# Performance work log

Hardware: AMD Instinct MI355X
Metric: run time of the kernel (lower is better)

The kernel has to match this reference:

```python
import jax, jax.numpy as jnp
import numpy as np

B, S, D = 4, 2048, 1024   # batch, seq_len, size
K = 4                     # max_choice
A = 2                     # activate_choice (== default forward choices)


def setup_inputs() -> dict:
    key = jax.random.key(0)
    ks = jax.random.split(key, 8)
    sc = 0.02  # weight init scale
    return {
        "x": jax.random.normal(ks[0], (B, S, D), jnp.float32),
        "Wm": jax.random.normal(ks[1], (A, D, D), jnp.float32) * sc,   # Memory expert weights
        "bm": jnp.zeros((A, D), jnp.float32),
        "ln_g": jnp.ones((D,), jnp.float32),                            # shared LayerNorm (self.lim)
        "ln_b": jnp.zeros((D,), jnp.float32),
        "Wg": jax.random.normal(ks[2], (D, K), jnp.float32) * sc,       # Linker gate
        "bg": jnp.zeros((K,), jnp.float32),
        "We": jax.random.normal(ks[3], (K, D, D), jnp.float32) * sc,    # Linker experts
        "be": jnp.zeros((K, D), jnp.float32),
        "Wfit": jax.random.normal(ks[4], ((A + 1) * D, D), jnp.float32) * sc,
        "bfit": jnp.zeros((D,), jnp.float32),
        "choices": A,
    }


def _layer_norm(x, g, b, eps=1e-5):
    m = jnp.mean(x, axis=-1, keepdims=True)
    v = jnp.mean((x - m) ** 2, axis=-1, keepdims=True)
    return (x - m) * jax.lax.rsqrt(v + eps) * g + b


def reference(x, Wm, bm, ln_g, ln_b, Wg, bg, We, be, Wfit, bfit, choices):
    # Triple-nested per-token loop vectorized: the in-place += means each
    # choice's Memory expert sees the x already updated by previous choices,
    # i.e. sequentially over `choices`: x <- x + LN(Memory_c(x)).
    for c in range(choices):
        mem = jnp.einsum('bsd,de->bse', x, Wm[c]) + bm[c]
        x = x + _layer_norm(mem, ln_g, ln_b)

    # Linker: gate over max_choice experts, pick top-`choices`, concat outputs.
    logits = jnp.einsum('bsd,dk->bsk', x, Wg) + bg          # [B,S,K]
    _, idx = jax.lax.top_k(logits, choices)                  # [B,S,A]
    eo = jnp.einsum('bsd,kde->bske', x, We) + be             # [B,S,K,D]
    sel = jnp.take_along_axis(eo, idx[..., None], axis=2)    # [B,S,A,D]
    link = sel.reshape(sel.shape[0], sel.shape[1], -1)       # [B,S,A*D]

    h = jnp.concatenate([link, x], axis=-1)                  # [B,S,(A+1)*D]
    h = jnp.einsum('bsf,fd->bsd', h, Wfit) + bfit
    h = _layer_norm(h, ln_g, ln_b)
    return jax.nn.gelu(h, approximate=False)
```

## Files before the change

### kernel.cpp

```cpp
#include <hip/hip_runtime.h>
#include <hip/hip_bf16.h>
#include <math.h>

typedef __bf16 bf16x8 __attribute__((ext_vector_type(8)));
typedef float  f32x4  __attribute__((ext_vector_type(4)));
typedef unsigned int   u32;
typedef unsigned short u16;
typedef u16 u16x8 __attribute__((ext_vector_type(8)));

#define D_ 1024
#define M_ 8192

static __device__ __forceinline__ u16 f2bf(float f) {
  u32 x = __float_as_uint(f);
  return (u16)((x + 0x7fffu + ((x >> 16) & 1u)) >> 16);
}
static __device__ __forceinline__ float bf2f(u16 s) {
  union { u32 b; float f; } u; u.b = ((u32)s) << 16; return u.f;
}
static __device__ __forceinline__ void gload16(const u16* g, u16* l) {
  __builtin_amdgcn_global_load_lds((const __attribute__((address_space(1))) u32*)g,
                                   (__attribute__((address_space(3))) u32*)l, 16, 0, 0);
}


__global__ __launch_bounds__(256) void pack_A_mem(const float* __restrict__ x, u16* __restrict__ dst) {
  int gid = blockIdx.x * 256 + threadIdx.x;
  int G = gid & 2047;
  int kblk = (gid >> 11) & 31;
  int mblk = gid >> 16;
  int rrow = G >> 3, gp = G & 7;
  int kg = gp ^ (rrow & 7);
  int region = kblk >> 4;
  int k = ((kblk & 15) * 8 + kg) * 8;
  const float* src = x + ((size_t)mblk * 256 + rrow) * D_ + k;
  f32x4 v0 = *reinterpret_cast<const f32x4*>(src);
  f32x4 v1 = *reinterpret_cast<const f32x4*>(src + 4);
  u16x8 o8;
#pragma unroll
  for (int j = 0; j < 4; ++j) {
    u16 h0 = f2bf(v0[j]); o8[j]     = region ? f2bf(v0[j] - bf2f(h0)) : h0;
    u16 h1 = f2bf(v1[j]); o8[4 + j] = region ? f2bf(v1[j] - bf2f(h1)) : h1;
  }
  *reinterpret_cast<u16x8*>(dst + (size_t)gid * 8) = o8;
}

__global__ __launch_bounds__(256) void pack_W_mem(const float* __restrict__ W, u16* __restrict__ dst) {
  __shared__ float tile[64][129];
  int bidx = blockIdx.x;
  int nt = bidx & 7, kt = (bidx >> 3) & 15, c = bidx >> 7;
  const float* Ws = W + ((size_t)c * D_ + kt * 64) * D_ + nt * 128;
#pragma unroll
  for (int rep = 0; rep < 32; ++rep) {
    int idx = rep * 256 + threadIdx.x;
    tile[idx >> 7][idx & 127] = Ws[(size_t)(idx >> 7) * D_ + (idx & 127)];
  }
  __syncthreads();
#pragma unroll
  for (int rep = 0; rep < 8; ++rep) {
    int gi = rep * 256 + threadIdx.x;
    int region = gi >> 10;
    int G = gi & 1023;
    int col = G >> 3, gp = G & 7;
    int kg = gp ^ (col & 7);
    u16x8 o8;
#pragma unroll
    for (int j = 0; j < 8; ++j) {
      float v = tile[kg * 8 + j][col];
      u16 h = f2bf(v);
      o8[j] = region ? f2bf(v - bf2f(h)) : h;
    }
    int kblk = region * 16 + kt;
    size_t off = ((((size_t)c * 8 + nt) * 32 + kblk) * 1024 + col * 8 + gp) * 8;
    *reinterpret_cast<u16x8*>(dst + off) = o8;
  }
}

__global__ __launch_bounds__(256) void pack_W_plain(const float* __restrict__ W, u16* __restrict__ dst, int KBLK) {
  __shared__ float tile[64][129];
  int bidx = blockIdx.x;
  int nt = bidx & 7;
  int t2 = bidx >> 3;
  int kt = t2 % KBLK;
  int e  = t2 / KBLK;
  const float* Ws = W + ((size_t)e * KBLK * 64 + kt * 64) * D_ + nt * 128;
#pragma unroll
  for (int rep = 0; rep < 32; ++rep) {
    int idx = rep * 256 + threadIdx.x;
    tile[idx >> 7][idx & 127] = Ws[(size_t)(idx >> 7) * D_ + (idx & 127)];
  }
  __syncthreads();
#pragma unroll
  for (int rep = 0; rep < 4; ++rep) {
    int gi = rep * 256 + threadIdx.x;
    int col = gi >> 3, gp = gi & 7;
    int kg = gp ^ (col & 7);
    u16x8 o8;
#pragma unroll
    for (int j = 0; j < 8; ++j) o8[j] = f2bf(tile[kg * 8 + j][col]);
    size_t off = ((((size_t)e * 8 + nt) * KBLK + kt) * 1024 + col * 8 + gp) * 8;
    *reinterpret_cast<u16x8*>(dst + off) = o8;
  }
}


__global__ __launch_bounds__(256) void ln1_pack(const float* __restrict__ xin, const float* __restrict__ mem,
                                                const float* __restrict__ bm, const float* __restrict__ g,
                                                const float* __restrict__ b, float* __restrict__ xout,
                                                u16* __restrict__ apack) {
  int row = blockIdx.x, tid = threadIdx.x;
  __shared__ float yrow[1024];
  __shared__ float red[8];
  f32x4 mv = *reinterpret_cast<const f32x4*>(mem + (size_t)row * D_ + tid * 4);
  f32x4 bi = *reinterpret_cast<const f32x4*>(bm + tid * 4);
  float a[4]; float s = 0.f, ss = 0.f;
#pragma unroll
  for (int i = 0; i < 4; ++i) { a[i] = mv[i] + bi[i]; s += a[i]; ss += a[i] * a[i]; }
#pragma unroll
  for (int o = 1; o < 64; o <<= 1) { s += __shfl_xor(s, o); ss += __shfl_xor(ss, o); }
  int wv = tid >> 6, ln = tid & 63;
  if (ln == 0) { red[wv] = s; red[4 + wv] = ss; }
  __syncthreads();
  float S = red[0] + red[1] + red[2] + red[3];
  float SS = red[4] + red[5] + red[6] + red[7];
  float mean = S * (1.f / 1024.f);
  float var = SS * (1.f / 1024.f) - mean * mean;
  float rs = rsqrtf(var + 1e-5f);
  f32x4 g4 = *reinterpret_cast<const f32x4*>(g + tid * 4);
  f32x4 b4 = *reinterpret_cast<const f32x4*>(b + tid * 4);
  f32x4 xv = *reinterpret_cast<const f32x4*>(xin + (size_t)row * D_ + tid * 4);
  f32x4 o4;
#pragma unroll
  for (int i = 0; i < 4; ++i) o4[i] = xv[i] + (a[i] - mean) * rs * g4[i] + b4[i];
  *reinterpret_cast<f32x4*>(xout + (size_t)row * D_ + tid * 4) = o4;
  *reinterpret_cast<f32x4*>(yrow + tid * 4) = o4;
  __syncthreads();
  int region = tid >> 7;
  int q = tid & 127;
  int kblk = region * 16 + (q >> 3);
  int kg = q & 7;
  int rrow = row & 255, mblk = row >> 8;
  const float* ys = yrow + q * 8;
  u16x8 o8;
#pragma unroll
  for (int j = 0; j < 8; ++j) {
    float v = ys[j]; u16 h = f2bf(v);
    o8[j] = region ? f2bf(v - bf2f(h)) : h;
  }
  size_t off = (((size_t)mblk * 32 + kblk) * 2048 + rrow * 8 + (kg ^ (rrow & 7))) * 8;
  *reinterpret_cast<u16x8*>(apack + off) = o8;
}

__global__ __launch_bounds__(256) void ln2_gate_pack(const float* __restrict__ xin, const float* __restrict__ mem,
                                                     const float* __restrict__ bm1, const float* __restrict__ g,
                                                     const float* __restrict__ b, const float* __restrict__ Wg,
                                                     const float* __restrict__ bg, u16* __restrict__ apack,
                                                     u16* __restrict__ hpack, int2* __restrict__ idx) {
  int row = blockIdx.x, tid = threadIdx.x;
  __shared__ float yrow[1024];
  __shared__ float red[8];
  __shared__ float gred[16];
  f32x4 mv = *reinterpret_cast<const f32x4*>(mem + (size_t)row * D_ + tid * 4);
  f32x4 bi = *reinterpret_cast<const f32x4*>(bm1 + tid * 4);
  float a[4]; float s = 0.f, ss = 0.f;
#pragma unroll
  for (int i = 0; i < 4; ++i) { a[i] = mv[i] + bi[i]; s += a[i]; ss += a[i] * a[i]; }
#pragma unroll
  for (int o = 1; o < 64; o <<= 1) { s += __shfl_xor(s, o); ss += __shfl_xor(ss, o); }
  int wv = tid >> 6, ln = tid & 63;
  if (ln == 0) { red[wv] = s; red[4 + wv] = ss; }
  __syncthreads();
  float S = red[0] + red[1] + red[2] + red[3];
  float SS = red[4] + red[5] + red[6] + red[7];
  float mean = S * (1.f / 1024.f);
  float var = SS * (1.f / 1024.f) - mean * mean;
  float rs = rsqrtf(var + 1e-5f);
  f32x4 g4 = *reinterpret_cast<const f32x4*>(g + tid * 4);
  f32x4 b4 = *reinterpret_cast<const f32x4*>(b + tid * 4);
  f32x4 xv = *reinterpret_cast<const f32x4*>(xin + (size_t)row * D_ + tid * 4);
  f32x4 o4;
#pragma unroll
  for (int i = 0; i < 4; ++i) o4[i] = xv[i] + (a[i] - mean) * rs * g4[i] + b4[i];
  *reinterpret_cast<f32x4*>(yrow + tid * 4) = o4;
  float p0 = 0.f, p1 = 0.f, p2 = 0.f, p3 = 0.f;
#pragma unroll
  for (int i = 0; i < 4; ++i) {
    f32x4 w = *reinterpret_cast<const f32x4*>(Wg + (size_t)(tid * 4 + i) * 4);
    p0 += o4[i] * w[0]; p1 += o4[i] * w[1]; p2 += o4[i] * w[2]; p3 += o4[i] * w[3];
  }
#pragma unroll
  for (int o = 1; o < 64; o <<= 1) {
    p0 += __shfl_xor(p0, o); p1 += __shfl_xor(p1, o);
    p2 += __shfl_xor(p2, o); p3 += __shfl_xor(p3, o);
  }
  if (ln == 0) { gred[wv * 4] = p0; gred[wv * 4 + 1] = p1; gred[wv * 4 + 2] = p2; gred[wv * 4 + 3] = p3; }
  __syncthreads();
  if (tid == 0) {
    float lg[4];
#pragma unroll
    for (int c = 0; c < 4; ++c) lg[c] = gred[c] + gred[4 + c] + gred[8 + c] + gred[12 + c] + bg[c];
    int i0 = 0; float v0 = lg[0];
#pragma unroll
    for (int k = 1; k < 4; ++k) if (lg[k] > v0) { v0 = lg[k]; i0 = k; }
    int i1 = -1; float v1 = -3.4e38f;
#pragma unroll
    for (int k = 0; k < 4; ++k) if (k != i0 && lg[k] > v1) { v1 = lg[k]; i1 = k; }
    idx[row] = make_int2(i0, i1);
  }
  int q = tid & 127;
  int kblk = q >> 3, kg = q & 7;
  int rrow = row & 255, mblk = row >> 8;
  const float* ys = yrow + q * 8;
  u16x8 o8;
#pragma unroll
  for (int j = 0; j < 8; ++j) o8[j] = f2bf(ys[j]);
  int pos = rrow * 8 + (kg ^ (rrow & 7));
  if (tid < 128) {
    *reinterpret_cast<u16x8*>(apack + (((size_t)mblk * 16 + kblk) * 2048 + pos) * 8) = o8;
  } else {
    *reinterpret_cast<u16x8*>(hpack + (((size_t)mblk * 48 + 32 + kblk) * 2048 + pos) * 8) = o8;
  }
}

__global__ __launch_bounds__(256) void final_ln_gelu(const float* __restrict__ fit, const float* __restrict__ bfit,
                                                     const float* __restrict__ g, const float* __restrict__ b,
                                                     float* __restrict__ out) {
  int row = blockIdx.x, tid = threadIdx.x;
  f32x4 hv = *reinterpret_cast<const f32x4*>(fit + (size_t)row * D_ + tid * 4);
  f32x4 bi = *reinterpret_cast<const f32x4*>(bfit + tid * 4);
  float a[4]; float s = 0.f, ss = 0.f;
#pragma unroll
  for (int i = 0; i < 4; ++i) { a[i] = hv[i] + bi[i]; s += a[i]; ss += a[i] * a[i]; }
#pragma unroll
  for (int o = 1; o < 64; o <<= 1) { s += __shfl_xor(s, o); ss += __shfl_xor(ss, o); }
  __shared__ float red[8];
  int wv = tid >> 6, ln = tid & 63;
  if (ln == 0) { red[wv] = s; red[4 + wv] = ss; }
  __syncthreads();
  float S = red[0] + red[1] + red[2] + red[3];
  float SS = red[4] + red[5] + red[6] + red[7];
  float mean = S * (1.f / 1024.f);
  float var = SS * (1.f / 1024.f) - mean * mean;
  float rs = rsqrtf(var + 1e-5f);
  f32x4 g4 = *reinterpret_cast<const f32x4*>(g + tid * 4);
  f32x4 b4 = *reinterpret_cast<const f32x4*>(b + tid * 4);
  f32x4 o4;
#pragma unroll
  for (int i = 0; i < 4; ++i) {
    float y = (a[i] - mean) * rs * g4[i] + b4[i];
    o4[i] = 0.5f * y * (1.f + erff(y * 0.70710678118654752f));
  }
  *reinterpret_cast<f32x4*>(out + (size_t)row * D_ + tid * 4) = o4;
}

#define MFMA(a, b, c) __builtin_amdgcn_mfma_f32_16x16x32_bf16(a, b, c, 0, 0, 0)

template<int MEMFOLD, int EPI>
__global__ __launch_bounds__(256, 2) void gemm4(const u16* __restrict__ A, const u16* __restrict__ B,
                                                float* __restrict__ C, u16* __restrict__ hp,
                                                const int2* __restrict__ idx, const float* __restrict__ be,
                                                int KIT, int AKB, int BKB) {
  __shared__ __align__(16) u16 lds[16384];
  const int tid = threadIdx.x;
  const int wid = tid >> 6, l = tid & 63;
  const int wm = wid >> 1, wn = wid & 1;
  const int lk = l >> 4, l15 = l & 15;
  const int bid = blockIdx.x;
  const int mblk = bid & 63;
  const int nblk = (bid >> 6) & 7;
  const int e    = bid >> 9;
  const int half = mblk & 1;

  const u16* Ablob = A + (size_t)(mblk >> 1) * AKB * 16384 + (size_t)half * 8192;
  const u16* Bblob = B + ((size_t)e * 8 + nblk) * BKB * 8192;

  f32x4 acc[4][4];
#pragma unroll
  for (int i = 0; i < 4; ++i)
#pragma unroll
    for (int j = 0; j < 4; ++j) acc[i][j] = (f32x4){0.f, 0.f, 0.f, 0.f};

  auto amap = [&](int it) -> int {
    if (!MEMFOLD) return it;
    int kb = (int)((unsigned)it / 3u), sub = it - kb * 3;
    return kb + (sub == 2 ? 16 : 0);
  };
  auto bmap = [&](int it) -> int {
    if (!MEMFOLD) return it;
    int kb = (int)((unsigned)it / 3u), sub = it - kb * 3;
    return kb + (sub == 1 ? 16 : 0);
  };

  auto ldA = [&](int mi, int ks) -> bf16x8 {
    int r = wm * 64 + mi * 16 + l15;
    int gp = (ks * 4 + lk) ^ (r & 7);
    return *reinterpret_cast<const bf16x8*>(&lds[(r * 8 + gp) * 8]);
  };
  auto ldB = [&](int ni, int ks) -> bf16x8 {
    int c = wn * 64 + ni * 16 + l15;
    int gp = (ks * 4 + lk) ^ (c & 7);
    return *reinterpret_cast<const bf16x8*>(&lds[8192 + (c * 8 + gp) * 8]);
  };

  for (int t = 0; t < KIT; ++t) {
    const u16* As = Ablob + (size_t)amap(t) * 16384;
    const u16* Bs = Bblob + (size_t)bmap(t) * 8192;
#pragma unroll
    for (int i = 0; i < 4; ++i) {
      int u = i * 256 + tid;
      gload16(As + (size_t)u * 8, &lds[u * 8]);
      gload16(Bs + (size_t)u * 8, &lds[8192 + u * 8]);
    }
    __syncthreads();
#pragma unroll
    for (int ks = 0; ks < 2; ++ks) {
      bf16x8 A0 = ldA(0, ks), A1 = ldA(1, ks), A2 = ldA(2, ks), A3 = ldA(3, ks);
      bf16x8 B0 = ldB(0, ks), B1 = ldB(1, ks), B2 = ldB(2, ks), B3 = ldB(3, ks);
      __builtin_amdgcn_s_setprio(1);
      acc[0][0] = MFMA(A0, B0, acc[0][0]); acc[1][0] = MFMA(A1, B0, acc[1][0]);
      acc[2][0] = MFMA(A2, B0, acc[2][0]); acc[3][0] = MFMA(A3, B0, acc[3][0]);
      acc[0][1] = MFMA(A0, B1, acc[0][1]); acc[1][1] = MFMA(A1, B1, acc[1][1]);
      acc[2][1] = MFMA(A2, B1, acc[2][1]); acc[3][1] = MFMA(A3, B1, acc[3][1]);
      acc[0][2] = MFMA(A0, B2, acc[0][2]); acc[1][2] = MFMA(A1, B2, acc[1][2]);
      acc[2][2] = MFMA(A2, B2, acc[2][2]); acc[3][2] = MFMA(A3, B2, acc[3][2]);
      acc[0][3] = MFMA(A0, B3, acc[0][3]); acc[1][3] = MFMA(A1, B3, acc[1][3]);
      acc[2][3] = MFMA(A2, B3, acc[2][3]); acc[3][3] = MFMA(A3, B3, acc[3][3]);
      __builtin_amdgcn_s_setprio(0);
    }
    __syncthreads();
  }

  if (EPI == 0) {
#pragma unroll
    for (int mi = 0; mi < 4; ++mi) {
#pragma unroll
      for (int jj = 0; jj < 4; ++jj) {
        int row = mblk * 128 + wm * 64 + mi * 16 + lk * 4 + jj;
        float* Crow = C + (size_t)row * D_ + nblk * 128 + wn * 64 + l15;
#pragma unroll
        for (int ni = 0; ni < 4; ++ni) Crow[ni * 16] = acc[mi][ni][jj];
      }
    }
  } else {
#pragma unroll
    for (int mi = 0; mi < 4; ++mi) {
      int rbase = mblk * 128 + wm * 64 + mi * 16 + lk * 4;
      int2 rid[4];
#pragma unroll
      for (int jj = 0; jj < 4; ++jj) rid[jj] = idx[rbase + jj];
#pragma unroll
      for (int ni = 0; ni < 4; ++ni) {
        int col = nblk * 128 + wn * 64 + ni * 16 + l15;
        float bev = be[(size_t)e * D_ + col];
#pragma unroll
        for (int jj = 0; jj < 4; ++jj) {
          int slot = (rid[jj].x == e) ? 0 : ((rid[jj].y == e) ? 1 : -1);
          if (slot >= 0) {
            int row = rbase + jj;
            int hmblk = row >> 8;
            int rrow = row & 255;
            int kh = slot * D_ + col;
            int kblk = kh >> 6;
            int kg = (kh >> 3) & 7;
            size_t off = (((size_t)hmblk * 48 + kblk) * 2048 + rrow * 8 + (kg ^ (rrow & 7))) * 8 + (kh & 7);
            hp[off] = f2bf(acc[mi][ni][jj] + bev);
          }
        }
      }
    }
  }
}

extern "C" void kernel_launch(void* const* d_in, const int* in_sizes, int n_in,
                              void* d_out, int out_size, void* d_ws, size_t ws_size,
                              hipStream_t stream) {
  const float* x_in = (const float*)d_in[0];
  const float* Wm   = (const float*)d_in[1];
  const float* bm   = (const float*)d_in[2];
  const float* ln_g = (const float*)d_in[3];
  const float* ln_b = (const float*)d_in[4];
  const float* Wg   = (const float*)d_in[5];
  const float* bg   = (const float*)d_in[6];
  const float* We   = (const float*)d_in[7];
  const float* be   = (const float*)d_in[8];
  const float* Wfit = (const float*)d_in[9];
  const float* bfit = (const float*)d_in[10];
  float* out = (float*)d_out;

  char* ws = (char*)d_ws;
  size_t off = 0;
  auto alloc = [&](size_t bytes) -> void* {
    void* p = ws + off; off += (bytes + 255) & ~(size_t)255; return p;
  };
  float* x1      = (float*)alloc((size_t)M_ * D_ * 4);
  float* memb    = (float*)alloc((size_t)M_ * D_ * 4);
  u16* AmemPack  = (u16*)alloc((size_t)32 * 32 * 2048 * 16);
  u16* AplainPk  = (u16*)alloc((size_t)32 * 16 * 2048 * 16);
  u16* Hpack     = (u16*)alloc((size_t)32 * 48 * 2048 * 16);
  u16* WmPack    = (u16*)alloc((size_t)2 * 8 * 32 * 1024 * 16);
  u16* WePack    = (u16*)alloc((size_t)4 * 8 * 16 * 1024 * 16);
  u16* WfPack    = (u16*)alloc((size_t)8 * 48 * 1024 * 16);
  int2* idxb     = (int2*)alloc((size_t)M_ * 8);

  pack_W_mem  <<<256, 256, 0, stream>>>(Wm, WmPack);
  pack_W_plain<<<512, 256, 0, stream>>>(We, WePack, 16);
  pack_W_plain<<<384, 256, 0, stream>>>(Wfit, WfPack, 48);

  pack_A_mem<<<8192, 256, 0, stream>>>(x_in, AmemPack);
  gemm4<1, 0><<<512, 256, 0, stream>>>(AmemPack, WmPack, memb, nullptr, nullptr, nullptr, 48, 32, 32);
  ln1_pack<<<8192, 256, 0, stream>>>(x_in, memb, bm, ln_g, ln_b, x1, AmemPack);
  gemm4<1, 0><<<512, 256, 0, stream>>>(AmemPack, WmPack + (size_t)2097152, memb,
                                       nullptr, nullptr, nullptr, 48, 32, 32);
  ln2_gate_pack<<<8192, 256, 0, stream>>>(x1, memb, bm + D_, ln_g, ln_b, Wg, bg, AplainPk, Hpack, idxb);

  gemm4<0, 1><<<2048, 256, 0, stream>>>(AplainPk, WePack, nullptr, Hpack, idxb, be, 16, 16, 16);

  gemm4<0, 0><<<512, 256, 0, stream>>>(Hpack, WfPack, memb, nullptr, nullptr, nullptr, 48, 48, 48);

  final_ln_gelu<<<8192, 256, 0, stream>>>(memb, bfit, ln_g, ln_b, out);
}
```

Measured before the change: 436.4 us.

## Split-K the non-expert GEMMs in two and sum partials in LayerNorm kernels

The memory GEMMs and the fit GEMM now run as split-K with two halves, doubling the grid from 512 to 1024 blocks. Each half writes a separate fp32 partial buffer, and the following LayerNorm kernels read and add both partials. This targets under-filled GPU occupancy, since 512 blocks is only about two per CU on MI355X. It also raises the launch-bounds occupancy hint to 4 and drops the s_setprio calls, at the cost of an extra 32 MB of partial-sum writes and reads per GEMM.

New measurement: 439.9 us. No clear change (+0.8%).

```diff
diff --git a/kernel.cpp b/kernel.cpp
--- a/kernel.cpp
+++ b/kernel.cpp
@@ -104,18 +104,19 @@
 }
 
 
-__global__ __launch_bounds__(256) void ln1_pack(const float* __restrict__ xin, const float* __restrict__ mem,
-                                                const float* __restrict__ bm, const float* __restrict__ g,
-                                                const float* __restrict__ b, float* __restrict__ xout,
-                                                u16* __restrict__ apack) {
+__global__ __launch_bounds__(256) void ln1_pack(const float* __restrict__ xin, const float* __restrict__ mem0,
+                                                const float* __restrict__ mem1, const float* __restrict__ bm,
+                                                const float* __restrict__ g, const float* __restrict__ b,
+                                                float* __restrict__ xout, u16* __restrict__ apack) {
   int row = blockIdx.x, tid = threadIdx.x;
   __shared__ float yrow[1024];
   __shared__ float red[8];
-  f32x4 mv = *reinterpret_cast<const f32x4*>(mem + (size_t)row * D_ + tid * 4);
+  f32x4 m0 = *reinterpret_cast<const f32x4*>(mem0 + (size_t)row * D_ + tid * 4);
+  f32x4 m1 = *reinterpret_cast<const f32x4*>(mem1 + (size_t)row * D_ + tid * 4);
   f32x4 bi = *reinterpret_cast<const f32x4*>(bm + tid * 4);
   float a[4]; float s = 0.f, ss = 0.f;
 #pragma unroll
-  for (int i = 0; i < 4; ++i) { a[i] = mv[i] + bi[i]; s += a[i]; ss += a[i] * a[i]; }
+  for (int i = 0; i < 4; ++i) { a[i] = m0[i] + m1[i] + bi[i]; s += a[i]; ss += a[i] * a[i]; }
 #pragma unroll
   for (int o = 1; o < 64; o <<= 1) { s += __shfl_xor(s, o); ss += __shfl_xor(ss, o); }
   int wv = tid >> 6, ln = tid & 63;
@@ -151,20 +152,22 @@
   *reinterpret_cast<u16x8*>(apack + off) = o8;
 }
 
-__global__ __launch_bounds__(256) void ln2_gate_pack(const float* __restrict__ xin, const float* __restrict__ mem,
-                                                     const float* __restrict__ bm1, const float* __restrict__ g,
-                                                     const float* __restrict__ b, const float* __restrict__ Wg,
-                                                     const float* __restrict__ bg, u16* __restrict__ apack,
-                                                     u16* __restrict__ hpack, int2* __restrict__ idx) {
+__global__ __launch_bounds__(256) void ln2_gate_pack(const float* __restrict__ xin, const float* __restrict__ mem0,
+                                                     const float* __restrict__ mem1, const float* __restrict__ bm1,
+                                                     const float* __restrict__ g, const float* __restrict__ b,
+                                                     const float* __restrict__ Wg, const float* __restrict__ bg,
+                                                     u16* __restrict__ apack, u16* __restrict__ hpack,
+                                                     int2* __restrict__ idx) {
   int row = blockIdx.x, tid = threadIdx.x;
   __shared__ float yrow[1024];
   __shared__ float red[8];
   __shared__ float gred[16];
-  f32x4 mv = *reinterpret_cast<const f32x4*>(mem + (size_t)row * D_ + tid * 4);
+  f32x4 m0 = *reinterpret_cast<const f32x4*>(mem0 + (size_t)row * D_ + tid * 4);
+  f32x4 m1 = *reinterpret_cast<const f32x4*>(mem1 + (size_t)row * D_ + tid * 4);
   f32x4 bi = *reinterpret_cast<const f32x4*>(bm1 + tid * 4);
   float a[4]; float s = 0.f, ss = 0.f;
 #pragma unroll
-  for (int i = 0; i < 4; ++i) { a[i] = mv[i] + bi[i]; s += a[i]; ss += a[i] * a[i]; }
+  for (int i = 0; i < 4; ++i) { a[i] = m0[i] + m1[i] + bi[i]; s += a[i]; ss += a[i] * a[i]; }
 #pragma unroll
   for (int o = 1; o < 64; o <<= 1) { s += __shfl_xor(s, o); ss += __shfl_xor(ss, o); }
   int wv = tid >> 6, ln = tid & 63;
@@ -222,15 +225,16 @@
   }
 }
 
-__global__ __launch_bounds__(256) void final_ln_gelu(const float* __restrict__ fit, const float* __restrict__ bfit,
-                                                     const float* __restrict__ g, const float* __restrict__ b,
-                                                     float* __restrict__ out) {
+__global__ __launch_bounds__(256) void final_ln_gelu(const float* __restrict__ fit0, const float* __restrict__ fit1,
+                                                     const float* __restrict__ bfit, const float* __restrict__ g,
+                                                     const float* __restrict__ b, float* __restrict__ out) {
   int row = blockIdx.x, tid = threadIdx.x;
-  f32x4 hv = *reinterpret_cast<const f32x4*>(fit + (size_t)row * D_ + tid * 4);
+  f32x4 h0 = *reinterpret_cast<const f32x4*>(fit0 + (size_t)row * D_ + tid * 4);
+  f32x4 h1 = *reinterpret_cast<const f32x4*>(fit1 + (size_t)row * D_ + tid * 4);
   f32x4 bi = *reinterpret_cast<const f32x4*>(bfit + tid * 4);
   float a[4]; float s = 0.f, ss = 0.f;
 #pragma unroll
-  for (int i = 0; i < 4; ++i) { a[i] = hv[i] + bi[i]; s += a[i]; ss += a[i] * a[i]; }
+  for (int i = 0; i < 4; ++i) { a[i] = h0[i] + h1[i] + bi[i]; s += a[i]; ss += a[i] * a[i]; }
 #pragma unroll
   for (int o = 1; o < 64; o <<= 1) { s += __shfl_xor(s, o); ss += __shfl_xor(ss, o); }
   __shared__ float red[8];
@@ -256,7 +260,7 @@
 #define MFMA(a, b, c) __builtin_amdgcn_mfma_f32_16x16x32_bf16(a, b, c, 0, 0, 0)
 
 template<int MEMFOLD, int EPI>
-__global__ __launch_bounds__(256, 2) void gemm4(const u16* __restrict__ A, const u16* __restrict__ B,
+__global__ __launch_bounds__(256, 4) void gemm4(const u16* __restrict__ A, const u16* __restrict__ B,
                                                 float* __restrict__ C, u16* __restrict__ hp,
                                                 const int2* __restrict__ idx, const float* __restrict__ be,
                                                 int KIT, int AKB, int BKB) {
@@ -272,7 +276,8 @@
   const int half = mblk & 1;
 
   const u16* Ablob = A + (size_t)(mblk >> 1) * AKB * 16384 + (size_t)half * 8192;
-  const u16* Bblob = B + ((size_t)e * 8 + nblk) * BKB * 8192;
+  const u16* Bblob = B + ((size_t)(EPI == 1 ? e : 0) * 8 + nblk) * BKB * 8192;
+  const int koff = (EPI == 0) ? e * KIT : 0;
 
   f32x4 acc[4][4];
 #pragma unroll
@@ -302,7 +307,8 @@
     return *reinterpret_cast<const bf16x8*>(&lds[8192 + (c * 8 + gp) * 8]);
   };
 
-  for (int t = 0; t < KIT; ++t) {
+  for (int tt = 0; tt < KIT; ++tt) {
+    int t = koff + tt;
     const u16* As = Ablob + (size_t)amap(t) * 16384;
     const u16* Bs = Bblob + (size_t)bmap(t) * 8192;
 #pragma unroll
@@ -316,7 +322,6 @@
     for (int ks = 0; ks < 2; ++ks) {
       bf16x8 A0 = ldA(0, ks), A1 = ldA(1, ks), A2 = ldA(2, ks), A3 = ldA(3, ks);
       bf16x8 B0 = ldB(0, ks), B1 = ldB(1, ks), B2 = ldB(2, ks), B3 = ldB(3, ks);
-      __builtin_amdgcn_s_setprio(1);
       acc[0][0] = MFMA(A0, B0, acc[0][0]); acc[1][0] = MFMA(A1, B0, acc[1][0]);
       acc[2][0] = MFMA(A2, B0, acc[2][0]); acc[3][0] = MFMA(A3, B0, acc[3][0]);
       acc[0][1] = MFMA(A0, B1, acc[0][1]); acc[1][1] = MFMA(A1, B1, acc[1][1]);
@@ -325,18 +330,18 @@
       acc[2][2] = MFMA(A2, B2, acc[2][2]); acc[3][2] = MFMA(A3, B2, acc[3][2]);
       acc[0][3] = MFMA(A0, B3, acc[0][3]); acc[1][3] = MFMA(A1, B3, acc[1][3]);
       acc[2][3] = MFMA(A2, B3, acc[2][3]); acc[3][3] = MFMA(A3, B3, acc[3][3]);
-      __builtin_amdgcn_s_setprio(0);
     }
     __syncthreads();
   }
 
   if (EPI == 0) {
+    float* Cp = C + (size_t)e * M_ * D_;
 #pragma unroll
     for (int mi = 0; mi < 4; ++mi) {
 #pragma unroll
       for (int jj = 0; jj < 4; ++jj) {
         int row = mblk * 128 + wm * 64 + mi * 16 + lk * 4 + jj;
-        float* Crow = C + (size_t)row * D_ + nblk * 128 + wn * 64 + l15;
+        float* Crow = Cp + (size_t)row * D_ + nblk * 128 + wn * 64 + l15;
 #pragma unroll
         for (int ni = 0; ni < 4; ++ni) Crow[ni * 16] = acc[mi][ni][jj];
       }
@@ -393,7 +398,7 @@
     void* p = ws + off; off += (bytes + 255) & ~(size_t)255; return p;
   };
   float* x1      = (float*)alloc((size_t)M_ * D_ * 4);
-  float* memb    = (float*)alloc((size_t)M_ * D_ * 4);
+  float* memb    = (float*)alloc((size_t)2 * M_ * D_ * 4);
   u16* AmemPack  = (u16*)alloc((size_t)32 * 32 * 2048 * 16);
   u16* AplainPk  = (u16*)alloc((size_t)32 * 16 * 2048 * 16);
   u16* Hpack     = (u16*)alloc((size_t)32 * 48 * 2048 * 16);
@@ -401,21 +406,23 @@
   u16* WePack    = (u16*)alloc((size_t)4 * 8 * 16 * 1024 * 16);
   u16* WfPack    = (u16*)alloc((size_t)8 * 48 * 1024 * 16);
   int2* idxb     = (int2*)alloc((size_t)M_ * 8);
+  float* memb2   = memb + (size_t)M_ * D_;
 
   pack_W_mem  <<<256, 256, 0, stream>>>(Wm, WmPack);
   pack_W_plain<<<512, 256, 0, stream>>>(We, WePack, 16);
   pack_W_plain<<<384, 256, 0, stream>>>(Wfit, WfPack, 48);
 
   pack_A_mem<<<8192, 256, 0, stream>>>(x_in, AmemPack);
-  gemm4<1, 0><<<512, 256, 0, stream>>>(AmemPack, WmPack, memb, nullptr, nullptr, nullptr, 48, 32, 32);
-  ln1_pack<<<8192, 256, 0, stream>>>(x_in, memb, bm, ln_g, ln_b, x1, AmemPack);
-  gemm4<1, 0><<<512, 256, 0, stream>>>(AmemPack, WmPack + (size_t)2097152, memb,
-                                       nullptr, nullptr, nullptr, 48, 32, 32);
-  ln2_gate_pack<<<8192, 256, 0, stream>>>(x1, memb, bm + D_, ln_g, ln_b, Wg, bg, AplainPk, Hpack, idxb);
+  gemm4<1, 0><<<1024, 256, 0, stream>>>(AmemPack, WmPack, memb, nullptr, nullptr, nullptr, 24, 32, 32);
+  ln1_pack<<<8192, 256, 0, stream>>>(x_in, memb, memb2, bm, ln_g, ln_b, x1, AmemPack);
+  gemm4<1, 0><<<1024, 256, 0, stream>>>(AmemPack, WmPack + (size_t)2097152, memb,
+                                        nullptr, nullptr, nullptr, 24, 32, 32);
+  ln2_gate_pack<<<8192, 256, 0, stream>>>(x1, memb, memb2, bm + D_, ln_g, ln_b, Wg, bg,
+                                          AplainPk, Hpack, idxb);
 
   gemm4<0, 1><<<2048, 256, 0, stream>>>(AplainPk, WePack, nullptr, Hpack, idxb, be, 16, 16, 16);
 
-  gemm4<0, 0><<<512, 256, 0, stream>>>(Hpack, WfPack, memb, nullptr, nullptr, nullptr, 48, 48, 48);
-
-  final_ln_gelu<<<8192, 256, 0, stream>>>(memb, bfit, ln_g, ln_b, out);
-}
+  gemm4<0, 0><<<1024, 256, 0, stream>>>(Hpack, WfPack, memb, nullptr, nullptr, nullptr, 24, 48, 48);
+
+  final_ln_gelu<<<8192, 256, 0, stream>>>(memb, memb2, bfit, ln_g, ln_b, out);
+}
```
